# Kernel tuning notes

Measured on AMD Instinct MI355X. Metric: run time of the kernel, lower is better.

## Reference

```python
import jax, jax.numpy as jnp
from jax import lax
import numpy as np

B, F, K = 2048, 4096, 64  # batch, features (output_size), channels (input_size)
ETA = 1.0  # Dirichlet hyperparameter eta


def setup_inputs() -> dict:
    key = jax.random.key(0)
    k1, k2, k3 = jax.random.split(key, 3)
    x = jax.random.randint(k1, (B, F), 0, 50).astype(jnp.int32)        # observed counts
    theta = jax.random.uniform(k2, (B, K), jnp.float32)                # latent rates (positive)
    phi = jax.random.uniform(k3, (K, F), jnp.float32)                  # unnormalized signatures
    return {"x": x, "theta": theta, "phi": phi}


def _augment_reduce(key, theta, phi, x):
    """Exact multinomial thinning chi_{ijk} ~ Mult(x_ij, theta_ik*phi_kj / sum_k)
    via K sequential conditional binomials; returns the scatter-reduced
    sufficient statistics m_ik = sum_j chi and x_jk = sum_i chi without ever
    materializing the (B, F, K) tensor."""
    Kc = theta.shape[1]
    n0 = x.astype(jnp.float32)                 # (B,F) remaining counts
    denom = theta @ phi                        # (B,F) total unnormalized prob mass
    keys = jax.random.split(key, Kc)

    def step(carry, inp):
        n_rem, den = carry
        kk, th_k, ph_k = inp                   # th_k: (B,), ph_k: (F,)
        p = th_k[:, None] * ph_k[None, :]      # (B,F) mass of channel k
        ratio = jnp.clip(p / jnp.maximum(den, 1e-30), 0.0, 1.0)
        chi = jax.random.binomial(kk, n_rem, ratio, dtype=jnp.float32)  # (B,F)
        return (n_rem - chi, den - p), (chi.sum(axis=1), chi.sum(axis=0))

    _, (m_cols, x_cols) = lax.scan(step, (n0, denom), (keys, theta.T, phi))
    m_ik = m_cols.T                            # (B,K)
    x_jk = x_cols.T                            # (F,K)
    return m_ik, x_jk


def reference(x, theta, phi):
    # phi rows live on the simplex (Dirichlet-distributed in the model)
    phi = phi / phi.sum(axis=-1, keepdims=True)
    key = jax.random.key(42)
    k_aug, k_dir = jax.random.split(key)
    m_ik, x_jk = _augment_reduce(k_aug, theta, phi, x)
    # phi ~ Dir(x_.jk + eta), row-wise over channels: alpha shape (K, F)
    alpha = x_jk.T + ETA
    phi_new = jax.random.dirichlet(k_dir, alpha, dtype=jnp.float32)
    return m_ik, phi_new
```

## Files before the change

kernel.cpp:

```cpp
#include <hip/hip_runtime.h>
#include <stdint.h>

#define BB 2048
#define FF 4096
#define KK 64

#define INV_DEPTH 50
#define BTRS_DEPTH 16
#define PARK_CAP 384

__host__ __device__ __forceinline__ uint32_t rotl32(uint32_t v, int n) {
  return (v << n) | (v >> (32 - n));
}

__host__ __device__ __forceinline__ void tf2x32(uint32_t key0, uint32_t key1,
                                                uint32_t c0, uint32_t c1,
                                                uint32_t& o0, uint32_t& o1) {
  uint32_t ks2 = key0 ^ key1 ^ 0x1BD11BDAu;
  uint32_t x0 = c0 + key0, x1 = c1 + key1;
#define TFR(r) { x0 += x1; x1 = rotl32(x1, (r)); x1 ^= x0; }
  TFR(13) TFR(15) TFR(26) TFR(6)
  x0 += key1; x1 += ks2 + 1u;
  TFR(17) TFR(29) TFR(16) TFR(24)
  x0 += ks2; x1 += key0 + 2u;
  TFR(13) TFR(15) TFR(26) TFR(6)
  x0 += key0; x1 += key1 + 3u;
  TFR(17) TFR(29) TFR(16) TFR(24)
  x0 += key1; x1 += ks2 + 4u;
  TFR(13) TFR(15) TFR(26) TFR(6)
  x0 += ks2; x1 += key0 + 5u;
#undef TFR
  o0 = x0; o1 = x1;
}

__host__ __device__ __forceinline__ void key_child(uint32_t k0, uint32_t k1, uint32_t idx,
                                                   uint32_t& o0, uint32_t& o1) {
  tf2x32(k0, k1, 0u, idx, o0, o1);
}

__device__ __forceinline__ uint32_t rbits(uint32_t k0, uint32_t k1, uint32_t e) {
  uint32_t a, b;
  tf2x32(k0, k1, 0u, e, a, b);
  return a ^ b;
}

__device__ __forceinline__ float u01_from_bits(uint32_t bits) {
  uint32_t fb = (bits >> 9) | 0x3f800000u;
  return __fsub_rn(__uint_as_float(fb), 1.0f);
}

__device__ __forceinline__ float erfinv_f32(float x) {
  float w = -log1pf(-__fmul_rn(x, x));
  float p;
  if (w < 5.0f) {
    w = __fsub_rn(w, 2.5f);
    p = 2.81022636e-08f;
    p = __fadd_rn(3.43273939e-07f, __fmul_rn(p, w));
    p = __fadd_rn(-3.5233877e-06f, __fmul_rn(p, w));
    p = __fadd_rn(-4.39150654e-06f, __fmul_rn(p, w));
    p = __fadd_rn(0.00021858087f, __fmul_rn(p, w));
    p = __fadd_rn(-0.00125372503f, __fmul_rn(p, w));
    p = __fadd_rn(-0.00417768164f, __fmul_rn(p, w));
    p = __fadd_rn(0.246640727f, __fmul_rn(p, w));
    p = __fadd_rn(1.50140941f, __fmul_rn(p, w));
  } else {
    w = __fsub_rn(sqrtf(w), 3.0f);
    p = -0.000200214257f;
    p = __fadd_rn(0.000100950558f, __fmul_rn(p, w));
    p = __fadd_rn(0.00134934322f, __fmul_rn(p, w));
    p = __fadd_rn(-0.00367342844f, __fmul_rn(p, w));
    p = __fadd_rn(0.00573950773f, __fmul_rn(p, w));
    p = __fadd_rn(-0.0076224613f, __fmul_rn(p, w));
    p = __fadd_rn(0.00943887047f, __fmul_rn(p, w));
    p = __fadd_rn(1.00167406f, __fmul_rn(p, w));
    p = __fadd_rn(2.83297682f, __fmul_rn(p, w));
  }
  return __fmul_rn(p, x);
}

__device__ __forceinline__ float normal_from_key(uint32_t k0, uint32_t k1) {
  float u01 = u01_from_bits(rbits(k0, k1, 0u));
  const float lo = -0.99999994f;
  float u = __fadd_rn(__fmul_rn(u01, 2.0f), lo);
  u = fmaxf(lo, u);
  return __fmul_rn(1.41421356f, erfinv_f32(u));
}

__device__ __forceinline__ float stirling_tail(float k) {
  const float tab[10] = {
    0.0810614667953272f, 0.0413406959554092f, 0.0276779256849983f,
    0.02079067210376509f, 0.0166446911898211f, 0.0138761288230707f,
    0.0118967099458917f, 0.0104112652619720f, 0.00925546218271273f,
    0.00833056343336287f};
  if (k <= 9.0f) return tab[(int)k];
  float kp1 = __fadd_rn(k, 1.0f);
  float kp1sq = __fmul_rn(kp1, kp1);
  float inner = __fsub_rn(0.0027777778f, 0.00079365081f / kp1sq);
  float t = __fsub_rn(0.083333336f, inner / kp1sq);
  return t / kp1;
}


__global__ void rowsum_kernel(const float* __restrict__ phi, float* __restrict__ rs) {
  __shared__ float red[256];
  int k = blockIdx.x;
  float s = 0.0f;
  for (int j = threadIdx.x; j < FF; j += 256) s += phi[k * FF + j];
  red[threadIdx.x] = s;
  __syncthreads();
  for (int off = 128; off > 0; off >>= 1) {
    if (threadIdx.x < off) red[threadIdx.x] += red[threadIdx.x + off];
    __syncthreads();
  }
  if (threadIdx.x == 0) rs[k] = red[0];
}

__global__ void chains_kernel(uint32_t ka0, uint32_t ka1, uint32_t* __restrict__ ch) {
  int k = threadIdx.x;
  if (k >= KK) return;
  uint32_t s0, s1;
  key_child(ka0, ka1, (uint32_t)k, s0, s1);

  uint2* inv = (uint2*)ch + k * INV_DEPTH;
  uint2* b0p = (uint2*)(ch + KK * INV_DEPTH * 2) + k * BTRS_DEPTH;
  uint2* b1p = (uint2*)(ch + KK * INV_DEPTH * 2 + KK * BTRS_DEPTH * 2) + k * BTRS_DEPTH;
  uint2* cont = (uint2*)(ch + KK * INV_DEPTH * 2 + KK * BTRS_DEPTH * 4) + k;

  uint32_t c0 = s0, c1 = s1;
  for (int t = 0; t < INV_DEPTH; ++t) {
    uint32_t a, b, n0, n1;
    key_child(c0, c1, 0u, a, b);
    key_child(c0, c1, 1u, n0, n1);
    inv[t] = make_uint2(a, b);
    c0 = n0; c1 = n1;
  }
  c0 = s0; c1 = s1;
  for (int t = 0; t < BTRS_DEPTH; ++t) {
    uint32_t n0, n1, a0, a1, u0, u1;
    key_child(c0, c1, 0u, n0, n1);
    key_child(c0, c1, 1u, a0, a1);
    key_child(c0, c1, 2u, u0, u1);
    b0p[t] = make_uint2(a0, a1);
    b1p[t] = make_uint2(u0, u1);
    c0 = n0; c1 = n1;
  }
  cont[0] = make_uint2(c0, c1);
}

__global__ __launch_bounds__(256) void sample_kernel(
    const int* __restrict__ xin, const float* __restrict__ theta,
    const float* __restrict__ phi, const float* __restrict__ rs,
    float* __restrict__ m_out, float* __restrict__ x_out,
    const uint32_t* __restrict__ ch) {
  __shared__ float phs[KK][64];
  __shared__ float xs[KK][64];
  __shared__ float denl[32][64];
  __shared__ float ml[32][64];
  __shared__ uint2 park[PARK_CAP];
  __shared__ int ctr, pk_n, pk_claim;

  const uint2* inv_all = (const uint2*)ch;
  const uint2* b0_all = (const uint2*)(ch + KK * INV_DEPTH * 2);
  const uint2* b1_all = (const uint2*)(ch + KK * INV_DEPTH * 2 + KK * BTRS_DEPTH * 2);
  const uint2* cont_all = (const uint2*)(ch + KK * INV_DEPTH * 2 + KK * BTRS_DEPTH * 4);

  int tid = threadIdx.x;
  int jt = blockIdx.x;
  int rg = blockIdx.y;
  int row0 = rg * 32;

  for (int idx = tid; idx < KK * 64; idx += 256) {
    int k = idx >> 6, jl = idx & 63;
    phs[k][jl] = phi[k * FF + jt * 64 + jl] / rs[k];
    xs[k][jl] = 0.0f;
  }
  for (int idx = tid; idx < 32 * 64; idx += 256) ml[idx >> 6][idx & 63] = 0.0f;
  if (tid == 0) { ctr = 0; pk_n = 0; pk_claim = 0; }
  __syncthreads();

  for (int s = tid; s < 32 * 64; s += 256) {
    int il = s >> 6, jl = s & 63;
    const float* tr = theta + (size_t)(row0 + il) * KK;
    float d = 0.0f;
    #pragma unroll 8
    for (int kk = 0; kk < KK; ++kk) d = fmaf(tr[kk], phs[kk][jl], d);
    denl[il][jl] = d;
  }
  __syncthreads();

  int mode;
  int il = 0, jje = 0, k = 0, ti = 0;
  uint32_t e = 0;
  bool plth = true;
  float n = 0, den = 0, p = 0, q = 0, l1p = 0, gs = 0, ng = 0;
  float sB = 0, sA = 0, sC = 0, sVr = 0, sR = 0, sAlf = 0, sMm = 0;

  mode = 3;
  for (int iter = 0; iter < 300000 && __any(mode != 4); ++iter) {
    if (mode == 3) {
      int tt = atomicAdd(&ctr, 1);
      if (tt >= 32 * 64) {
        mode = 4;
      } else {
        il = tt >> 6; jje = tt & 63;
        int gi = row0 + il, gj = jt * 64 + jje;
        n = (float)xin[gi * FF + gj];
        den = denl[il][jje];
        e = (uint32_t)(gi * FF + gj);
        k = 0;
        mode = 2;
      }
    }
    if (mode == 2) {
      float th = theta[(row0 + il) * KK + k];
      p = __fmul_rn(th, phs[k][jje]);
      float ratio = p / fmaxf(den, 1e-30f);
      ratio = fminf(fmaxf(ratio, 0.0f), 1.0f);
      plth = ratio < 0.5f;
      q = plth ? ratio : __fsub_rn(1.0f, ratio);
      if (n <= 0.0f || q <= 0.0f) {
        float chi = plth ? 0.0f : n;
        if (chi != 0.0f) {
          atomicAdd(&ml[il][k], chi);
          atomicAdd(&xs[k][jje], chi);
        }
        mode = 3;
      } else if (__fmul_rn(n, q) <= 10.0f) {
        l1p = log1pf(-q);
        gs = 0.0f; ng = 0.0f; ti = 0;
        mode = 0;
      } else {
        int slot = atomicAdd(&pk_n, 1);
        if (slot < PARK_CAP) {
          park[slot] = make_uint2((uint32_t)il | ((uint32_t)jje << 5) |
                                  ((uint32_t)k << 11) | ((uint32_t)(int)n << 17),
                                  __float_as_uint(den));
          mode = 3;
        } else {
          float stddev = sqrtf(__fmul_rn(__fmul_rn(n, q), __fsub_rn(1.0f, q)));
          sB = __fadd_rn(1.15f, __fmul_rn(2.53f, stddev));
          sA = __fadd_rn(__fadd_rn(-0.0873f, __fmul_rn(0.0248f, sB)), __fmul_rn(0.01f, q));
          sC = __fadd_rn(__fmul_rn(n, q), 0.5f);
          sVr = __fsub_rn(0.92f, 4.2f / sB);
          sR = q / __fsub_rn(1.0f, q);
          sAlf = __fmul_rn(__fadd_rn(2.83f, 5.1f / sB), stddev);
          sMm = floorf(__fmul_rn(__fadd_rn(n, 1.0f), q));
          ti = 0;
          mode = 1;
        }
      }
    }
    if (mode == 0) {
      uint2 sk = inv_all[k * INV_DEPTH + ti];
      ng = __fadd_rn(ng, 1.0f);
      float u = u01_from_bits(rbits(sk.x, sk.y, e));
      float g = ceilf(logf(u) / l1p);
      gs = __fadd_rn(gs, g);
      ti++;
      if (!(gs <= n)) {
        float samp = __fsub_rn(ng, 1.0f);
        float chi = plth ? samp : __fsub_rn(n, samp);
        if (chi != 0.0f) {
          atomicAdd(&ml[il][k], chi);
          atomicAdd(&xs[k][jje], chi);
        }
        n = __fsub_rn(n, chi);
        den = __fsub_rn(den, p);
        k++;
        mode = (n <= 0.0f || k >= KK) ? 3 : 2;
      }
    }
    if (mode == 1) {
      uint32_t s00, s01, s10, s11;
      if (ti < BTRS_DEPTH) {
        uint2 A = b0_all[k * BTRS_DEPTH + ti];
        uint2 Bv = b1_all[k * BTRS_DEPTH + ti];
        s00 = A.x; s01 = A.y; s10 = Bv.x; s11 = Bv.y;
      } else {
        uint2 cc = cont_all[k];
        uint32_t c0 = cc.x, c1 = cc.y;
        for (int tw = BTRS_DEPTH; tw < ti; ++tw) {
          uint32_t a, b; key_child(c0, c1, 0u, a, b); c0 = a; c1 = b;
        }
        key_child(c0, c1, 1u, s00, s01);
        key_child(c0, c1, 2u, s10, s11);
      }
      float u = u01_from_bits(rbits(s00, s01, e));
      float v = u01_from_bits(rbits(s10, s11, e));
      u = __fsub_rn(u, 0.5f);
      float us = __fsub_rn(0.5f, fabsf(u));
      bool accept1 = (us >= 0.07f) && (v <= sVr);
      float kf = floorf(__fadd_rn(__fmul_rn(__fadd_rn(__fmul_rn(2.0f, sA) / us, sB), u), sC));
      bool reject = (kf < 0.0f) || (kf > n);
      float v2 = logf(__fmul_rn(v, sAlf) / __fadd_rn(sA / __fmul_rn(us, us), sB));
      float ub =
        __fadd_rn(
          __fadd_rn(
            __fadd_rn(
              __fmul_rn(__fadd_rn(sMm, 0.5f), logf(__fadd_rn(sMm, 1.0f) / __fmul_rn(sR, __fadd_rn(__fsub_rn(n, sMm), 1.0f)))),
              __fmul_rn(__fadd_rn(n, 1.0f), logf(__fadd_rn(__fsub_rn(n, sMm), 1.0f) / __fadd_rn(__fsub_rn(n, kf), 1.0f)))),
            __fmul_rn(__fadd_rn(kf, 0.5f), logf(__fmul_rn(sR, __fadd_rn(__fsub_rn(n, kf), 1.0f)) / __fadd_rn(kf, 1.0f)))),
          __fsub_rn(__fsub_rn(__fadd_rn(stirling_tail(sMm), stirling_tail(__fsub_rn(n, sMm))),
                              stirling_tail(kf)),
                    stirling_tail(__fsub_rn(n, kf))));
      bool accept2 = v2 <= ub;
      ti++;
      bool done2 = accept1 || ((!reject) && accept2);
      float samp = done2 ? kf : -1.0f;
      if (done2 || ti >= 64) {
        float chi = plth ? samp : __fsub_rn(n, samp);
        if (chi != 0.0f) {
          atomicAdd(&ml[il][k], chi);
          atomicAdd(&xs[k][jje], chi);
        }
        n = __fsub_rn(n, chi);
        den = __fsub_rn(den, p);
        k++;
        mode = (n <= 0.0f || k >= KK) ? 3 : 2;
      }
    }
  }

  __syncthreads();

  int pk_total = min(pk_n, PARK_CAP);
  mode = 3;
  for (int iter = 0; iter < 300000 && __any(mode != 4); ++iter) {
    if (mode == 3) {
      int tt = atomicAdd(&pk_claim, 1);
      if (tt >= pk_total) {
        mode = 4;
      } else {
        uint2 st = park[tt];
        il = (int)(st.x & 31u);
        jje = (int)((st.x >> 5) & 63u);
        k = (int)((st.x >> 11) & 63u);
        n = (float)(int)((st.x >> 17) & 63u);
        den = __uint_as_float(st.y);
        e = (uint32_t)((row0 + il) * FF + (jt * 64 + jje));
        mode = 2;
      }
    }
    if (mode == 2) {
      float th = theta[(row0 + il) * KK + k];
      p = __fmul_rn(th, phs[k][jje]);
      float ratio = p / fmaxf(den, 1e-30f);
      ratio = fminf(fmaxf(ratio, 0.0f), 1.0f);
      plth = ratio < 0.5f;
      q = plth ? ratio : __fsub_rn(1.0f, ratio);
      if (n <= 0.0f || q <= 0.0f) {
        float chi = plth ? 0.0f : n;
        if (chi != 0.0f) {
          atomicAdd(&ml[il][k], chi);
          atomicAdd(&xs[k][jje], chi);
        }
        mode = 3;
      } else if (__fmul_rn(n, q) <= 10.0f) {
        l1p = log1pf(-q);
        gs = 0.0f; ng = 0.0f; ti = 0;
        mode = 0;
      } else {
        float stddev = sqrtf(__fmul_rn(__fmul_rn(n, q), __fsub_rn(1.0f, q)));
        sB = __fadd_rn(1.15f, __fmul_rn(2.53f, stddev));
        sA = __fadd_rn(__fadd_rn(-0.0873f, __fmul_rn(0.0248f, sB)), __fmul_rn(0.01f, q));
        sC = __fadd_rn(__fmul_rn(n, q), 0.5f);
        sVr = __fsub_rn(0.92f, 4.2f / sB);
        sR = q / __fsub_rn(1.0f, q);
        sAlf = __fmul_rn(__fadd_rn(2.83f, 5.1f / sB), stddev);
        sMm = floorf(__fmul_rn(__fadd_rn(n, 1.0f), q));
        ti = 0;
        mode = 1;
      }
    }
    if (mode == 0) {
      uint2 sk = inv_all[k * INV_DEPTH + ti];
      ng = __fadd_rn(ng, 1.0f);
      float u = u01_from_bits(rbits(sk.x, sk.y, e));
      float g = ceilf(logf(u) / l1p);
      gs = __fadd_rn(gs, g);
      ti++;
      if (!(gs <= n)) {
        float samp = __fsub_rn(ng, 1.0f);
        float chi = plth ? samp : __fsub_rn(n, samp);
        if (chi != 0.0f) {
          atomicAdd(&ml[il][k], chi);
          atomicAdd(&xs[k][jje], chi);
        }
        n = __fsub_rn(n, chi);
        den = __fsub_rn(den, p);
        k++;
        mode = (n <= 0.0f || k >= KK) ? 3 : 2;
      }
    }
    if (mode == 1) {
      uint32_t s00, s01, s10, s11;
      if (ti < BTRS_DEPTH) {
        uint2 A = b0_all[k * BTRS_DEPTH + ti];
        uint2 Bv = b1_all[k * BTRS_DEPTH + ti];
        s00 = A.x; s01 = A.y; s10 = Bv.x; s11 = Bv.y;
      } else {
        uint2 cc = cont_all[k];
        uint32_t c0 = cc.x, c1 = cc.y;
        for (int tw = BTRS_DEPTH; tw < ti; ++tw) {
          uint32_t a, b; key_child(c0, c1, 0u, a, b); c0 = a; c1 = b;
        }
        key_child(c0, c1, 1u, s00, s01);
        key_child(c0, c1, 2u, s10, s11);
      }
      float u = u01_from_bits(rbits(s00, s01, e));
      float v = u01_from_bits(rbits(s10, s11, e));
      u = __fsub_rn(u, 0.5f);
      float us = __fsub_rn(0.5f, fabsf(u));
      bool accept1 = (us >= 0.07f) && (v <= sVr);
      float kf = floorf(__fadd_rn(__fmul_rn(__fadd_rn(__fmul_rn(2.0f, sA) / us, sB), u), sC));
      bool reject = (kf < 0.0f) || (kf > n);
      float v2 = logf(__fmul_rn(v, sAlf) / __fadd_rn(sA / __fmul_rn(us, us), sB));
      float ub =
        __fadd_rn(
          __fadd_rn(
            __fadd_rn(
              __fmul_rn(__fadd_rn(sMm, 0.5f), logf(__fadd_rn(sMm, 1.0f) / __fmul_rn(sR, __fadd_rn(__fsub_rn(n, sMm), 1.0f)))),
              __fmul_rn(__fadd_rn(n, 1.0f), logf(__fadd_rn(__fsub_rn(n, sMm), 1.0f) / __fadd_rn(__fsub_rn(n, kf), 1.0f)))),
            __fmul_rn(__fadd_rn(kf, 0.5f), logf(__fmul_rn(sR, __fadd_rn(__fsub_rn(n, kf), 1.0f)) / __fadd_rn(kf, 1.0f)))),
          __fsub_rn(__fsub_rn(__fadd_rn(stirling_tail(sMm), stirling_tail(__fsub_rn(n, sMm))),
                              stirling_tail(kf)),
                    stirling_tail(__fsub_rn(n, kf))));
      bool accept2 = v2 <= ub;
      ti++;
      bool done2 = accept1 || ((!reject) && accept2);
      float samp = done2 ? kf : -1.0f;
      if (done2 || ti >= 64) {
        float chi = plth ? samp : __fsub_rn(n, samp);
        if (chi != 0.0f) {
          atomicAdd(&ml[il][k], chi);
          atomicAdd(&xs[k][jje], chi);
        }
        n = __fsub_rn(n, chi);
        den = __fsub_rn(den, p);
        k++;
        mode = (n <= 0.0f || k >= KK) ? 3 : 2;
      }
    }
  }

  __syncthreads();
  for (int idx = tid; idx < 32 * 64; idx += 256) {
    int il2 = idx >> 6, k2 = idx & 63;
    float v = ml[il2][k2];
    if (v != 0.0f) atomicAdd(&m_out[(row0 + il2) * KK + k2], v);
  }
  for (int idx = tid; idx < KK * 64; idx += 256) {
    int k2 = idx >> 6, jl = idx & 63;
    float v = xs[k2][jl];
    if (v != 0.0f) atomicAdd(&x_out[k2 * FF + jt * 64 + jl], v);
  }
}

__global__ void gamma_kernel(float* __restrict__ xphi, uint32_t kd0, uint32_t kd1) {
  int e = blockIdx.x * blockDim.x + threadIdx.x;
  if (e >= KK * FF) return;
  float alpha = __fadd_rn(xphi[e], 1.0f);

  uint32_t k0, k1;
  key_child(kd0, kd1, (uint32_t)e, k0, k1);

  uint32_t nk0, nk1;
  key_child(k0, k1, 0u, nk0, nk1);
  k0 = nk0; k1 = nk1;

  float d = __fsub_rn(alpha, 0.33333334f);
  float cc = 0.33333334f / sqrtf(__fmul_rn(9.0f, d));

  float X = 0.0f, V = 1.0f, U = 2.0f;
  for (int t = 0; t < 256; ++t) {
    bool c1 = U >= __fsub_rn(1.0f, __fmul_rn(0.0331f, __fmul_rn(X, X)));
    bool c2 = logf(U) >= __fadd_rn(__fmul_rn(X, 0.5f),
                                   __fmul_rn(d, __fadd_rn(__fsub_rn(1.0f, V), logf(V))));
    if (!(c1 && c2)) break;
    uint32_t b0, b1, xk0, xk1, Uk0, Uk1;
    key_child(k0, k1, 0u, b0, b1);
    key_child(k0, k1, 1u, xk0, xk1);
    key_child(k0, k1, 2u, Uk0, Uk1);
    k0 = b0; k1 = b1;
    float x = 0.0f, v = -1.0f;
    uint32_t ik0 = xk0, ik1 = xk1;
    for (int s = 0; s < 16 && v <= 0.0f; ++s) {
      uint32_t n2a, n2b, sb0, sb1;
      key_child(ik0, ik1, 0u, n2a, n2b);
      key_child(ik0, ik1, 1u, sb0, sb1);
      ik0 = n2a; ik1 = n2b;
      x = normal_from_key(sb0, sb1);
      v = __fadd_rn(1.0f, __fmul_rn(x, cc));
    }
    X = __fmul_rn(x, x);
    V = __fmul_rn(__fmul_rn(v, v), v);
    U = u01_from_bits(rbits(Uk0, Uk1, 0u));
  }
  xphi[e] = __fadd_rn(logf(d), logf(V));
}

__global__ void rownorm_kernel(float* __restrict__ lg) {
  __shared__ float red[256];
  int k = blockIdx.x;
  float* p = lg + (size_t)k * FF;
  float mx = -INFINITY;
  for (int j = threadIdx.x; j < FF; j += 256) mx = fmaxf(mx, p[j]);
  red[threadIdx.x] = mx;
  __syncthreads();
  for (int off = 128; off > 0; off >>= 1) {
    if (threadIdx.x < off) red[threadIdx.x] = fmaxf(red[threadIdx.x], red[threadIdx.x + off]);
    __syncthreads();
  }
  mx = red[0];
  __syncthreads();
  float s = 0.0f;
  for (int j = threadIdx.x; j < FF; j += 256) s += expf(__fsub_rn(p[j], mx));
  red[threadIdx.x] = s;
  __syncthreads();
  for (int off = 128; off > 0; off >>= 1) {
    if (threadIdx.x < off) red[threadIdx.x] += red[threadIdx.x + off];
    __syncthreads();
  }
  float lse = __fadd_rn(logf(red[0]), mx);
  __syncthreads();
  for (int j = threadIdx.x; j < FF; j += 256) p[j] = expf(__fsub_rn(p[j], lse));
}

extern "C" void kernel_launch(void* const* d_in, const int* in_sizes, int n_in,
                              void* d_out, int out_size, void* d_ws, size_t ws_size,
                              hipStream_t stream) {
  (void)in_sizes; (void)n_in; (void)ws_size;
  const int* xin = (const int*)d_in[0];
  const float* theta = (const float*)d_in[1];
  const float* phi = (const float*)d_in[2];
  float* out = (float*)d_out;
  float* m_out = out;
  float* xphi = out + (size_t)BB * KK;
  float* rs = (float*)d_ws;
  uint32_t* chains = (uint32_t*)d_ws + 64;

  uint32_t ka0, ka1, kd0, kd1;
  tf2x32(0u, 42u, 0u, 0u, ka0, ka1);
  tf2x32(0u, 42u, 0u, 1u, kd0, kd1);

  hipMemsetAsync(d_out, 0, (size_t)out_size * sizeof(float), stream);
  hipLaunchKernelGGL(rowsum_kernel, dim3(KK), dim3(256), 0, stream, phi, rs);
  hipLaunchKernelGGL(chains_kernel, dim3(1), dim3(64), 0, stream, ka0, ka1, chains);
  hipLaunchKernelGGL(sample_kernel, dim3(64, 64), dim3(256), 0, stream,
                     xin, theta, phi, rs, m_out, xphi, chains);
  hipLaunchKernelGGL(gamma_kernel, dim3((KK * FF) / 256), dim3(256), 0, stream, xphi, kd0, kd1);
  hipLaunchKernelGGL(rownorm_kernel, dim3(KK), dim3(256), 0, stream, xphi);
}
```

Before: 5.495 ms.

## Use larger 1024-thread blocks with packed 16-bit integer shared-memory accumulators

Each sampling block now covers 128 rows with 1024 threads instead of 32 rows with 256 threads, and the park capacity grows. The float shared atomics for the m and x partial sums are replaced by integer atomics on pairs of 16-bit counters packed into 32-bit words, which halves the accumulator footprint. Work items are also assigned with a diagonal row rotation to spread shared-memory bank and atomic contention. The larger blocks cut the number of global atomic flushes and repeated per-block setup, but the packed counters could overflow if a count exceeds 65535, and 1024-thread blocks reduce scheduling flexibility and make threads wait longer for stragglers.

After: 4.477 ms (median of 2 runs). 18.5% less time.

```diff
diff --git a/kernel.cpp b/kernel.cpp
--- a/kernel.cpp
+++ b/kernel.cpp
@@ -7,7 +7,8 @@
 
 #define INV_DEPTH 50
 #define BTRS_DEPTH 16
-#define PARK_CAP 384
+#define ROWS 128
+#define PARK_CAP 512
 
 __host__ __device__ __forceinline__ uint32_t rotl32(uint32_t v, int n) {
   return (v << n) | (v >> (32 - n));
@@ -147,15 +148,15 @@
   cont[0] = make_uint2(c0, c1);
 }
 
-__global__ __launch_bounds__(256) void sample_kernel(
+__global__ __launch_bounds__(1024, 8) void sample_kernel(
     const int* __restrict__ xin, const float* __restrict__ theta,
     const float* __restrict__ phi, const float* __restrict__ rs,
     float* __restrict__ m_out, float* __restrict__ x_out,
     const uint32_t* __restrict__ ch) {
   __shared__ float phs[KK][64];
-  __shared__ float xs[KK][64];
-  __shared__ float denl[32][64];
-  __shared__ float ml[32][64];
+  __shared__ uint32_t xsp[KK][32];
+  __shared__ float denl[ROWS][64];
+  __shared__ uint32_t mlp[ROWS][32];
   __shared__ uint2 park[PARK_CAP];
   __shared__ int ctr, pk_n, pk_claim;
 
@@ -167,18 +168,18 @@
   int tid = threadIdx.x;
   int jt = blockIdx.x;
   int rg = blockIdx.y;
-  int row0 = rg * 32;
-
-  for (int idx = tid; idx < KK * 64; idx += 256) {
+  int row0 = rg * ROWS;
+
+  for (int idx = tid; idx < KK * 64; idx += 1024) {
     int k = idx >> 6, jl = idx & 63;
     phs[k][jl] = phi[k * FF + jt * 64 + jl] / rs[k];
-    xs[k][jl] = 0.0f;
-  }
-  for (int idx = tid; idx < 32 * 64; idx += 256) ml[idx >> 6][idx & 63] = 0.0f;
+  }
+  for (int idx = tid; idx < KK * 32; idx += 1024) xsp[idx >> 5][idx & 31] = 0u;
+  for (int idx = tid; idx < ROWS * 32; idx += 1024) mlp[idx >> 5][idx & 31] = 0u;
   if (tid == 0) { ctr = 0; pk_n = 0; pk_claim = 0; }
   __syncthreads();
 
-  for (int s = tid; s < 32 * 64; s += 256) {
+  for (int s = tid; s < ROWS * 64; s += 1024) {
     int il = s >> 6, jl = s & 63;
     const float* tr = theta + (size_t)(row0 + il) * KK;
     float d = 0.0f;
@@ -188,21 +189,23 @@
   }
   __syncthreads();
 
-  int mode;
+  int mode = 3;
   int il = 0, jje = 0, k = 0, ti = 0;
+  int jsh = 0;
   uint32_t e = 0;
   bool plth = true;
   float n = 0, den = 0, p = 0, q = 0, l1p = 0, gs = 0, ng = 0;
   float sB = 0, sA = 0, sC = 0, sVr = 0, sR = 0, sAlf = 0, sMm = 0;
 
-  mode = 3;
   for (int iter = 0; iter < 300000 && __any(mode != 4); ++iter) {
     if (mode == 3) {
       int tt = atomicAdd(&ctr, 1);
-      if (tt >= 32 * 64) {
+      if (tt >= ROWS * 64) {
         mode = 4;
       } else {
-        il = tt >> 6; jje = tt & 63;
+        jje = tt & 63;
+        il = ((tt >> 6) + jje) & (ROWS - 1);
+        jsh = (jje & 1) << 4;
         int gi = row0 + il, gj = jt * 64 + jje;
         n = (float)xin[gi * FF + gj];
         den = denl[il][jje];
@@ -221,8 +224,9 @@
       if (n <= 0.0f || q <= 0.0f) {
         float chi = plth ? 0.0f : n;
         if (chi != 0.0f) {
-          atomicAdd(&ml[il][k], chi);
-          atomicAdd(&xs[k][jje], chi);
+          uint32_t c = (uint32_t)(int)chi;
+          atomicAdd(&mlp[il][k >> 1], c << ((k & 1) << 4));
+          atomicAdd(&xsp[k][jje >> 1], c << jsh);
         }
         mode = 3;
       } else if (__fmul_rn(n, q) <= 10.0f) {
@@ -232,8 +236,8 @@
       } else {
         int slot = atomicAdd(&pk_n, 1);
         if (slot < PARK_CAP) {
-          park[slot] = make_uint2((uint32_t)il | ((uint32_t)jje << 5) |
-                                  ((uint32_t)k << 11) | ((uint32_t)(int)n << 17),
+          park[slot] = make_uint2((uint32_t)il | ((uint32_t)jje << 7) |
+                                  ((uint32_t)k << 13) | ((uint32_t)(int)n << 19),
                                   __float_as_uint(den));
           mode = 3;
         } else {
@@ -261,8 +265,9 @@
         float samp = __fsub_rn(ng, 1.0f);
         float chi = plth ? samp : __fsub_rn(n, samp);
         if (chi != 0.0f) {
-          atomicAdd(&ml[il][k], chi);
-          atomicAdd(&xs[k][jje], chi);
+          uint32_t c = (uint32_t)(int)chi;
+          atomicAdd(&mlp[il][k >> 1], c << ((k & 1) << 4));
+          atomicAdd(&xsp[k][jje >> 1], c << jsh);
         }
         n = __fsub_rn(n, chi);
         den = __fsub_rn(den, p);
@@ -310,8 +315,9 @@
       if (done2 || ti >= 64) {
         float chi = plth ? samp : __fsub_rn(n, samp);
         if (chi != 0.0f) {
-          atomicAdd(&ml[il][k], chi);
-          atomicAdd(&xs[k][jje], chi);
+          uint32_t c = (uint32_t)(int)chi;
+          atomicAdd(&mlp[il][k >> 1], c << ((k & 1) << 4));
+          atomicAdd(&xsp[k][jje >> 1], c << jsh);
         }
         n = __fsub_rn(n, chi);
         den = __fsub_rn(den, p);
@@ -332,11 +338,12 @@
         mode = 4;
       } else {
         uint2 st = park[tt];
-        il = (int)(st.x & 31u);
-        jje = (int)((st.x >> 5) & 63u);
-        k = (int)((st.x >> 11) & 63u);
-        n = (float)(int)((st.x >> 17) & 63u);
+        il = (int)(st.x & 127u);
+        jje = (int)((st.x >> 7) & 63u);
+        k = (int)((st.x >> 13) & 63u);
+        n = (float)(int)((st.x >> 19) & 63u);
         den = __uint_as_float(st.y);
+        jsh = (jje & 1) << 4;
         e = (uint32_t)((row0 + il) * FF + (jt * 64 + jje));
         mode = 2;
       }
@@ -351,8 +358,9 @@
       if (n <= 0.0f || q <= 0.0f) {
         float chi = plth ? 0.0f : n;
         if (chi != 0.0f) {
-          atomicAdd(&ml[il][k], chi);
-          atomicAdd(&xs[k][jje], chi);
+          uint32_t c = (uint32_t)(int)chi;
+          atomicAdd(&mlp[il][k >> 1], c << ((k & 1) << 4));
+          atomicAdd(&xsp[k][jje >> 1], c << jsh);
         }
         mode = 3;
       } else if (__fmul_rn(n, q) <= 10.0f) {
@@ -383,8 +391,9 @@
         float samp = __fsub_rn(ng, 1.0f);
         float chi = plth ? samp : __fsub_rn(n, samp);
         if (chi != 0.0f) {
-          atomicAdd(&ml[il][k], chi);
-          atomicAdd(&xs[k][jje], chi);
+          uint32_t c = (uint32_t)(int)chi;
+          atomicAdd(&mlp[il][k >> 1], c << ((k & 1) << 4));
+          atomicAdd(&xsp[k][jje >> 1], c << jsh);
         }
         n = __fsub_rn(n, chi);
         den = __fsub_rn(den, p);
@@ -432,8 +441,9 @@
       if (done2 || ti >= 64) {
         float chi = plth ? samp : __fsub_rn(n, samp);
         if (chi != 0.0f) {
-          atomicAdd(&ml[il][k], chi);
-          atomicAdd(&xs[k][jje], chi);
+          uint32_t c = (uint32_t)(int)chi;
+          atomicAdd(&mlp[il][k >> 1], c << ((k & 1) << 4));
+          atomicAdd(&xsp[k][jje >> 1], c << jsh);
         }
         n = __fsub_rn(n, chi);
         den = __fsub_rn(den, p);
@@ -444,15 +454,19 @@
   }
 
   __syncthreads();
-  for (int idx = tid; idx < 32 * 64; idx += 256) {
-    int il2 = idx >> 6, k2 = idx & 63;
-    float v = ml[il2][k2];
-    if (v != 0.0f) atomicAdd(&m_out[(row0 + il2) * KK + k2], v);
-  }
-  for (int idx = tid; idx < KK * 64; idx += 256) {
-    int k2 = idx >> 6, jl = idx & 63;
-    float v = xs[k2][jl];
-    if (v != 0.0f) atomicAdd(&x_out[k2 * FF + jt * 64 + jl], v);
+  for (int idx = tid; idx < ROWS * 32; idx += 1024) {
+    int il2 = idx >> 5, kp = idx & 31;
+    uint32_t v = mlp[il2][kp];
+    float lo = (float)(v & 0xFFFFu), hi = (float)(v >> 16);
+    if (lo != 0.0f) atomicAdd(&m_out[(row0 + il2) * KK + kp * 2], lo);
+    if (hi != 0.0f) atomicAdd(&m_out[(row0 + il2) * KK + kp * 2 + 1], hi);
+  }
+  for (int idx = tid; idx < KK * 32; idx += 1024) {
+    int k2 = idx >> 5, jp = idx & 31;
+    uint32_t v = xsp[k2][jp];
+    float lo = (float)(v & 0xFFFFu), hi = (float)(v >> 16);
+    if (lo != 0.0f) atomicAdd(&x_out[k2 * FF + jt * 64 + jp * 2], lo);
+    if (hi != 0.0f) atomicAdd(&x_out[k2 * FF + jt * 64 + jp * 2 + 1], hi);
   }
 }
 
@@ -546,7 +560,7 @@
   hipMemsetAsync(d_out, 0, (size_t)out_size * sizeof(float), stream);
   hipLaunchKernelGGL(rowsum_kernel, dim3(KK), dim3(256), 0, stream, phi, rs);
   hipLaunchKernelGGL(chains_kernel, dim3(1), dim3(64), 0, stream, ka0, ka1, chains);
-  hipLaunchKernelGGL(sample_kernel, dim3(64, 64), dim3(256), 0, stream,
+  hipLaunchKernelGGL(sample_kernel, dim3(64, BB / ROWS), dim3(1024), 0, stream,
                      xin, theta, phi, rs, m_out, xphi, chains);
   hipLaunchKernelGGL(gamma_kernel, dim3((KK * FF) / 256), dim3(256), 0, stream, xphi, kd0, kd1);
   hipLaunchKernelGGL(rownorm_kernel, dim3(KK), dim3(256), 0, stream, xphi);
```
